# Kernel tuning notes

Hardware: AMD Instinct MI355X
Metric: run time of the kernel (lower is better)

Reference implementation:

```python
import jax, jax.numpy as jnp
import numpy as np

HEADS = 16
DIM_HEAD = 64
MAX_FREQ = 256.0  # lucidrains RotaryEmbedding(freqs_for='pixel', max_freq=256)


def axial_freqs(H, W, dim_head):
    # per-axis rotary dim = dim_head // 2 (RotaryEmbedding(dim=head_dim//2))
    d = dim_head // 2
    base = jnp.linspace(1.0, MAX_FREQ / 2.0, d // 2) * jnp.pi  # (d/2,)

    def axis(n):
        pos = jnp.linspace(-1.0, 1.0, n)              # pixel positions
        f = pos[:, None] * base                        # (n, d/2)
        return jnp.repeat(f, 2, axis=-1)               # (n, d) interleaved pairs

    fh = jnp.broadcast_to(axis(H)[:, None, :], (H, W, d))
    fw = jnp.broadcast_to(axis(W)[None, :, :], (H, W, d))
    return jnp.concatenate([fh, fw], axis=-1)          # (H, W, dim_head)


def apply_rope(t, freqs):
    # t: (B,T,H,W,h,d); freqs: (H,W,d)
    f = freqs[:, :, None, :]                           # broadcast over heads
    x = t.reshape(t.shape[:-1] + (t.shape[-1] // 2, 2))
    x1, x2 = x[..., 0], x[..., 1]
    rot = jnp.stack([-x2, x1], axis=-1).reshape(t.shape)  # rotate_half (interleaved)
    return t * jnp.cos(f) + rot * jnp.sin(f)


def setup_inputs() -> dict:
    key = jax.random.key(0)
    k1, k2, k3 = jax.random.split(key, 3)
    B, T, H, W, D = 1, 8, 32, 32, 1024
    inner = HEADS * DIM_HEAD
    x = jax.random.normal(k1, (B, T, H, W, D), dtype=jnp.float32)
    Wqkv = jax.random.normal(k2, (D, 3 * inner), dtype=jnp.float32) * 0.02
    Wout = jax.random.normal(k3, (inner, D), dtype=jnp.float32) * 0.02
    bout = jnp.zeros((D,), dtype=jnp.float32)
    return {"x": x, "Wqkv": Wqkv, "Wout": Wout, "bout": bout}


def reference(x, Wqkv, Wout, bout):
    B, T, H, W, D = x.shape
    qkv = x @ Wqkv                                     # (B,T,H,W,3*inner)
    q, k, v = jnp.split(qkv, 3, axis=-1)
    shp = (B, T, H, W, HEADS, DIM_HEAD)
    q, k, v = q.reshape(shp), k.reshape(shp), v.reshape(shp)
    freqs = axial_freqs(H, W, DIM_HEAD)
    q = apply_rope(q, freqs)
    k = apply_rope(k, freqs)
    S = H * W
    q = q.reshape(B * T, S, HEADS, DIM_HEAD)
    k = k.reshape(B * T, S, HEADS, DIM_HEAD)
    v = v.reshape(B * T, S, HEADS, DIM_HEAD)
    scale = 1.0 / np.sqrt(DIM_HEAD).astype(np.float32)
    att = jnp.einsum('bshd,bthd->bhst', q, k) * scale  # (BT, h, S, S)
    att = jax.nn.softmax(att, axis=-1)
    o = jnp.einsum('bhst,bthd->bshd', att, v)          # (BT, S, h, d)
    o = o.reshape(B, T, H, W, HEADS * DIM_HEAD)
    return o @ Wout + bout
```

## Files before the change

kernel.cpp:

```cpp
#include <hip/hip_runtime.h>
#include <math.h>

#define DMODEL 1024
#define NQKV   3072
#define SEQ    1024
#define NH     16
#define DH     64
#define HS     (SEQ*DH)
constexpr float PI_F   = 3.14159265358979323846f;
constexpr float LOG2E  = 1.44269504088896f;

typedef _Float16 half8   __attribute__((ext_vector_type(8)));
typedef _Float16 half4   __attribute__((ext_vector_type(4)));
typedef float    floatx4 __attribute__((ext_vector_type(4)));

__device__ __forceinline__ void gload_lds16(const _Float16* g, _Float16* l) {
    __builtin_amdgcn_global_load_lds(
        (const __attribute__((address_space(1))) unsigned int*)g,
        (__attribute__((address_space(3)))       unsigned int*)l,
        16, 0, 0);
}

__global__ __launch_bounds__(256) void cvt_f16(
    const float* __restrict__ in, _Float16* __restrict__ out, int n)
{
    int i = (blockIdx.x*256 + threadIdx.x)*8;
    if (i >= n) return;
    float4 a = *(const float4*)(in + i);
    float4 b = *(const float4*)(in + i + 4);
    half8 h;
    h[0]=(_Float16)a.x; h[1]=(_Float16)a.y; h[2]=(_Float16)a.z; h[3]=(_Float16)a.w;
    h[4]=(_Float16)b.x; h[5]=(_Float16)b.y; h[6]=(_Float16)b.z; h[7]=(_Float16)b.w;
    *(half8*)(out + i) = h;
}

__global__ __launch_bounds__(256) void tr_cvt(
    const float* __restrict__ in, _Float16* __restrict__ out, int R, int C)
{
    __shared__ float T[32][33];
    const int bx = blockIdx.x, by = blockIdx.y;
    const int tx = threadIdx.x & 31, ty = threadIdx.x >> 5;
#pragma unroll
    for (int i = 0; i < 4; ++i)
        T[ty + i*8][tx] = in[(size_t)(by*32 + ty + i*8)*C + bx*32 + tx];
    __syncthreads();
#pragma unroll
    for (int i = 0; i < 4; ++i)
        out[(size_t)(bx*32 + ty + i*8)*R + by*32 + tx] = (_Float16)T[tx][ty + i*8];
}

__global__ __launch_bounds__(512) void gemm1_f16(
    const _Float16* __restrict__ A, const _Float16* __restrict__ Bt,
    _Float16* __restrict__ C, int M, int N, int K)
{
    __shared__ _Float16 As[2][2][4096] __attribute__((aligned(16)));
    __shared__ _Float16 Bs[2][2][8192] __attribute__((aligned(16)));

    const int tid  = threadIdx.x;
    const int w    = tid >> 6, lane = tid & 63, quad = lane >> 4, l = lane & 15;
    const int wm   = (w >> 2)*64, wn = (w & 3)*64;

    int bid = blockIdx.y*gridDim.x + blockIdx.x;
    const int per = (gridDim.x*gridDim.y) >> 3;
    bid = (bid & 7)*per + (bid >> 3);
    const int bx = bid % gridDim.x, by = bid / gridDim.x;
    const int m0 = by*128, n0 = bx*256;

    const int rs   = tid >> 2;
    const int csrc = (tid & 3) ^ ((tid >> 3) & 3);
    const _Float16* ga = A  + (size_t)(m0 + rs)*K + csrc*8;
    const _Float16* gb = Bt + (size_t)(n0 + rs)*K + csrc*8;
    const int swz8 = (quad ^ ((l >> 1) & 3))*8;

    floatx4 acc[4][4];
#pragma unroll
    for (int i = 0; i < 4; ++i)
#pragma unroll
        for (int j = 0; j < 4; ++j)
#pragma unroll
            for (int r = 0; r < 4; ++r) acc[i][j][r] = 0.f;

    gload_lds16(ga,                        &As[0][0][w*512]);
    gload_lds16(gb,                        &Bs[0][0][w*512]);
    gload_lds16(gb + (size_t)128*K,        &Bs[0][0][4096 + w*512]);
    gload_lds16(ga + 32,                   &As[0][1][w*512]);
    gload_lds16(gb + 32,                   &Bs[0][1][w*512]);
    gload_lds16(gb + 32 + (size_t)128*K,   &Bs[0][1][4096 + w*512]);

    const int KT = K / 64;
    for (int kt = 0; kt < KT; ++kt) {
        const int cur = kt & 1, nxt = cur ^ 1;
        const bool pf = (kt + 1 < KT);
        const size_t ko = (size_t)(kt + 1)*64;
        half8 af[4], bf[4];

        if (pf) gload_lds16(ga + ko, &As[nxt][0][w*512]);
        if (pf) { asm volatile("s_waitcnt vmcnt(4)" ::: "memory"); }
        else    { asm volatile("s_waitcnt vmcnt(3)" ::: "memory"); }
        __builtin_amdgcn_s_barrier();
        __builtin_amdgcn_sched_barrier(0);
#pragma unroll
        for (int mt = 0; mt < 4; ++mt)
            af[mt] = *(half8*)&As[cur][0][(wm + mt*16 + l)*32 + swz8];
#pragma unroll
        for (int nt = 0; nt < 4; ++nt)
            bf[nt] = *(half8*)&Bs[cur][0][(wn + nt*16 + l)*32 + swz8];
        if (pf) {
            gload_lds16(gb + ko,                 &Bs[nxt][0][w*512]);
            gload_lds16(gb + ko + (size_t)128*K, &Bs[nxt][0][4096 + w*512]);
        }
        asm volatile("s_waitcnt lgkmcnt(0)" ::: "memory");
        __builtin_amdgcn_sched_barrier(0);
        __builtin_amdgcn_s_setprio(1);
#pragma unroll
        for (int mt = 0; mt < 4; ++mt)
#pragma unroll
            for (int nt = 0; nt < 4; ++nt)
                acc[mt][nt] = __builtin_amdgcn_mfma_f32_16x16x32_f16(af[mt], bf[nt], acc[mt][nt], 0, 0, 0);
        __builtin_amdgcn_s_setprio(0);

        if (pf) gload_lds16(ga + ko + 32, &As[nxt][1][w*512]);
        if (pf) { asm volatile("s_waitcnt vmcnt(4)" ::: "memory"); }
        else    { asm volatile("s_waitcnt vmcnt(0)" ::: "memory"); }
        __builtin_amdgcn_s_barrier();
        __builtin_amdgcn_sched_barrier(0);
#pragma unroll
        for (int mt = 0; mt < 4; ++mt)
            af[mt] = *(half8*)&As[cur][1][(wm + mt*16 + l)*32 + swz8];
#pragma unroll
        for (int nt = 0; nt < 4; ++nt)
            bf[nt] = *(half8*)&Bs[cur][1][(wn + nt*16 + l)*32 + swz8];
        if (pf) {
            gload_lds16(gb + ko + 32,                 &Bs[nxt][1][w*512]);
            gload_lds16(gb + ko + 32 + (size_t)128*K, &Bs[nxt][1][4096 + w*512]);
        }
        asm volatile("s_waitcnt lgkmcnt(0)" ::: "memory");
        __builtin_amdgcn_sched_barrier(0);
        __builtin_amdgcn_s_setprio(1);
#pragma unroll
        for (int mt = 0; mt < 4; ++mt)
#pragma unroll
            for (int nt = 0; nt < 4; ++nt)
                acc[mt][nt] = __builtin_amdgcn_mfma_f32_16x16x32_f16(af[mt], bf[nt], acc[mt][nt], 0, 0, 0);
        __builtin_amdgcn_s_setprio(0);
    }

#pragma unroll
    for (int mt = 0; mt < 4; ++mt)
#pragma unroll
        for (int r = 0; r < 4; ++r) {
            size_t row = m0 + wm + mt*16 + quad*4 + r;
#pragma unroll
            for (int nt = 0; nt < 4; ++nt)
                C[row*N + n0 + wn + nt*16 + l] = (_Float16)acc[mt][nt][r];
        }
}

__global__ __launch_bounds__(512) void gemm2_f16(
    const _Float16* __restrict__ A, const _Float16* __restrict__ Bt,
    const float* __restrict__ bias, float* __restrict__ C, int M, int N, int K)
{
    __shared__ _Float16 As[2][2][4096] __attribute__((aligned(16)));
    __shared__ _Float16 Bs[2][2][8192] __attribute__((aligned(16)));

    const int tid  = threadIdx.x;
    const int w    = tid >> 6, lane = tid & 63, quad = lane >> 4, l = lane & 15;
    const int wm   = (w >> 2)*64, wn = (w & 3)*64;

    int bid = blockIdx.y*gridDim.x + blockIdx.x;
    const int per = (gridDim.x*gridDim.y) >> 3;
    bid = (bid & 7)*per + (bid >> 3);
    const int bx = bid % gridDim.x, by = bid / gridDim.x;
    const int m0 = by*128, n0 = bx*256;

    const int rs   = tid >> 2;
    const int csrc = (tid & 3) ^ ((tid >> 3) & 3);
    const _Float16* ga = A  + (size_t)(m0 + rs)*K + csrc*8;
    const _Float16* gb = Bt + (size_t)(n0 + rs)*K + csrc*8;
    const int swz8 = (quad ^ ((l >> 1) & 3))*8;

    floatx4 acc[4][4];
#pragma unroll
    for (int i = 0; i < 4; ++i)
#pragma unroll
        for (int j = 0; j < 4; ++j)
#pragma unroll
            for (int r = 0; r < 4; ++r) acc[i][j][r] = 0.f;

    gload_lds16(ga,                        &As[0][0][w*512]);
    gload_lds16(gb,                        &Bs[0][0][w*512]);
    gload_lds16(gb + (size_t)128*K,        &Bs[0][0][4096 + w*512]);
    gload_lds16(ga + 32,                   &As[0][1][w*512]);
    gload_lds16(gb + 32,                   &Bs[0][1][w*512]);
    gload_lds16(gb + 32 + (size_t)128*K,   &Bs[0][1][4096 + w*512]);

    const int KT = K / 64;
    for (int kt = 0; kt < KT; ++kt) {
        const int cur = kt & 1, nxt = cur ^ 1;
        const bool pf = (kt + 1 < KT);
        const size_t ko = (size_t)(kt + 1)*64;
        half8 af[4], bf[4];

        if (pf) gload_lds16(ga + ko, &As[nxt][0][w*512]);
        if (pf) { asm volatile("s_waitcnt vmcnt(4)" ::: "memory"); }
        else    { asm volatile("s_waitcnt vmcnt(3)" ::: "memory"); }
        __builtin_amdgcn_s_barrier();
        __builtin_amdgcn_sched_barrier(0);
#pragma unroll
        for (int mt = 0; mt < 4; ++mt)
            af[mt] = *(half8*)&As[cur][0][(wm + mt*16 + l)*32 + swz8];
#pragma unroll
        for (int nt = 0; nt < 4; ++nt)
            bf[nt] = *(half8*)&Bs[cur][0][(wn + nt*16 + l)*32 + swz8];
        if (pf) {
            gload_lds16(gb + ko,                 &Bs[nxt][0][w*512]);
            gload_lds16(gb + ko + (size_t)128*K, &Bs[nxt][0][4096 + w*512]);
        }
        asm volatile("s_waitcnt lgkmcnt(0)" ::: "memory");
        __builtin_amdgcn_sched_barrier(0);
        __builtin_amdgcn_s_setprio(1);
#pragma unroll
        for (int mt = 0; mt < 4; ++mt)
#pragma unroll
            for (int nt = 0; nt < 4; ++nt)
                acc[mt][nt] = __builtin_amdgcn_mfma_f32_16x16x32_f16(af[mt], bf[nt], acc[mt][nt], 0, 0, 0);
        __builtin_amdgcn_s_setprio(0);

        if (pf) gload_lds16(ga + ko + 32, &As[nxt][1][w*512]);
        if (pf) { asm volatile("s_waitcnt vmcnt(4)" ::: "memory"); }
        else    { asm volatile("s_waitcnt vmcnt(0)" ::: "memory"); }
        __builtin_amdgcn_s_barrier();
        __builtin_amdgcn_sched_barrier(0);
#pragma unroll
        for (int mt = 0; mt < 4; ++mt)
            af[mt] = *(half8*)&As[cur][1][(wm + mt*16 + l)*32 + swz8];
#pragma unroll
        for (int nt = 0; nt < 4; ++nt)
            bf[nt] = *(half8*)&Bs[cur][1][(wn + nt*16 + l)*32 + swz8];
        if (pf) {
            gload_lds16(gb + ko + 32,                 &Bs[nxt][1][w*512]);
            gload_lds16(gb + ko + 32 + (size_t)128*K, &Bs[nxt][1][4096 + w*512]);
        }
        asm volatile("s_waitcnt lgkmcnt(0)" ::: "memory");
        __builtin_amdgcn_sched_barrier(0);
        __builtin_amdgcn_s_setprio(1);
#pragma unroll
        for (int mt = 0; mt < 4; ++mt)
#pragma unroll
            for (int nt = 0; nt < 4; ++nt)
                acc[mt][nt] = __builtin_amdgcn_mfma_f32_16x16x32_f16(af[mt], bf[nt], acc[mt][nt], 0, 0, 0);
        __builtin_amdgcn_s_setprio(0);
    }

#pragma unroll
    for (int mt = 0; mt < 4; ++mt)
#pragma unroll
        for (int r = 0; r < 4; ++r) {
            size_t row = m0 + wm + mt*16 + quad*4 + r;
#pragma unroll
            for (int nt = 0; nt < 4; ++nt) {
                int col = n0 + wn + nt*16 + l;
                C[row*N + col] = acc[mt][nt][r] + bias[col];
            }
        }
}

__global__ __launch_bounds__(256) void rope_scatter(
    const _Float16* __restrict__ qkv,
    _Float16* __restrict__ qw, _Float16* __restrict__ kw,
    _Float16* __restrict__ vt)
{
    const int sc = blockIdx.x;
    const int bh = blockIdx.y;
    const int bt = bh >> 4, head = bh & 15;
    const int s0 = sc*64;
    const int tid = threadIdx.x;
    const int d0 = (tid & 7)*8;

    __shared__ _Float16 T[64][80];

#pragma unroll
    for (int half = 0; half < 2; ++half) {
        const int r = (tid >> 3) + half*32;
        const int s = s0 + r;
        const _Float16* src = qkv + (size_t)(bt*SEQ + s)*NQKV + head*DH + d0;
        half8 hq = *(const half8*)(src);
        half8 hk = *(const half8*)(src + DMODEL);
        half8 hv = *(const half8*)(src + 2*DMODEL);
        float fq[8], fk[8];
#pragma unroll
        for (int j = 0; j < 8; ++j) { fq[j] = (float)hq[j]; fk[j] = (float)hk[j]; }
        const int hp = s >> 5, wp = s & 31;
        const float ph = -1.0f + hp*(2.0f/31.0f);
        const float pw = -1.0f + wp*(2.0f/31.0f);
#pragma unroll
        for (int p = 0; p < 4; ++p) {
            int pg = (d0 >> 1) + p;
            float pos = (pg < 16) ? ph : pw;
            int   gi  = (pg < 16) ? pg : (pg - 16);
            float th  = pos * ((1.0f + gi*(127.0f/15.0f)) * PI_F);
            float sn, cs;
            sincosf(th, &sn, &cs);
            float q1 = fq[2*p], q2 = fq[2*p+1];
            fq[2*p]   = q1*cs - q2*sn;
            fq[2*p+1] = q2*cs + q1*sn;
            float k1 = fk[2*p], k2 = fk[2*p+1];
            fk[2*p]   = k1*cs - k2*sn;
            fk[2*p+1] = k2*cs + k1*sn;
        }
        half8 oq, ok;
        const float qsc = 0.125f * LOG2E;
#pragma unroll
        for (int j = 0; j < 8; ++j) {
            oq[j] = (_Float16)(fq[j]*qsc);
            ok[j] = (_Float16)fk[j];
        }
        *(half8*)(qw + (size_t)bh*HS + (size_t)s*DH + d0) = oq;
        *(half8*)(kw + (size_t)bh*HS + (size_t)s*DH + d0) = ok;
#pragma unroll
        for (int j = 0; j < 8; ++j) T[d0 + j][r] = hv[j];
    }
    __syncthreads();
    const int d = tid >> 2, so = (tid & 3)*16;
    half8 v0 = *(half8*)&T[d][so];
    half8 v1 = *(half8*)&T[d][so + 8];
    _Float16* dst = vt + (size_t)bh*HS + (size_t)d*SEQ + s0 + so;
    *(half8*)dst       = v0;
    *(half8*)(dst + 8) = v1;
}

#define BC  64
#define LDH 68

__global__ __launch_bounds__(256) void attn_mfma(
    const _Float16* __restrict__ qw, const _Float16* __restrict__ kw,
    const _Float16* __restrict__ vt, _Float16* __restrict__ om)
{
    const int qc = blockIdx.x;
    const int bh = blockIdx.y;
    const int tid  = threadIdx.x;
    const int w    = tid >> 6;
    const int lane = tid & 63;
    const int quad = lane >> 4;
    const int l    = lane & 15;

    __shared__ _Float16 Ks[2][BC][LDH];
    __shared__ _Float16 Vs[2][DH][LDH];
    __shared__ _Float16 Ps[4][32][LDH];
    __shared__ float    Ls[4][32];

    const _Float16* qp = qw + (size_t)bh*HS + (size_t)(qc*128 + w*32)*DH;
    const _Float16* kp = kw + (size_t)bh*HS;
    const _Float16* vp = vt + (size_t)bh*HS;

    half8 qf[2][2];
#pragma unroll
    for (int qt = 0; qt < 2; ++qt) {
        qf[qt][0] = *(const half8*)(qp + (size_t)(qt*16 + l)*DH + quad*8);
        qf[qt][1] = *(const half8*)(qp + (size_t)(qt*16 + l)*DH + quad*8 + 32);
    }

    const int rs = tid >> 3;
    const int cs = (tid & 7)*8;

    half8 kr0 = *(const half8*)(kp + (size_t)rs*DH + cs);
    half8 kr1 = *(const half8*)(kp + (size_t)(rs+32)*DH + cs);
    half8 vr0 = *(const half8*)(vp + (size_t)rs*SEQ + cs);
    half8 vr1 = *(const half8*)(vp + (size_t)(rs+32)*SEQ + cs);
    *(half8*)&Ks[0][rs][cs]    = kr0;
    *(half8*)&Ks[0][rs+32][cs] = kr1;
    *(half8*)&Vs[0][rs][cs]    = vr0;
    *(half8*)&Vs[0][rs+32][cs] = vr1;

    floatx4 Of[2][4];
#pragma unroll
    for (int qt = 0; qt < 2; ++qt)
#pragma unroll
        for (int dt = 0; dt < 4; ++dt)
#pragma unroll
            for (int r = 0; r < 4; ++r) Of[qt][dt][r] = 0.f;
    float lsum[2] = {0.f, 0.f};

    __syncthreads();

    for (int kc = 0; kc < SEQ/BC; ++kc) {
        const int cur = kc & 1;
        if (kc < SEQ/BC - 1) {
            const _Float16* kn = kp + (size_t)(kc+1)*BC*DH;
            const _Float16* vn = vp + (size_t)(kc+1)*BC;
            kr0 = *(const half8*)(kn + (size_t)rs*DH + cs);
            kr1 = *(const half8*)(kn + (size_t)(rs+32)*DH + cs);
            vr0 = *(const half8*)(vn + (size_t)rs*SEQ + cs);
            vr1 = *(const half8*)(vn + (size_t)(rs+32)*SEQ + cs);
        }

        floatx4 Sf[2][4];
#pragma unroll
        for (int kg = 0; kg < 4; ++kg) {
            half8 af0 = *(half8*)&Ks[cur][kg*16 + l][quad*8];
            half8 af1 = *(half8*)&Ks[cur][kg*16 + l][quad*8 + 32];
#pragma unroll
            for (int qt = 0; qt < 2; ++qt) {
                floatx4 a;
#pragma unroll
                for (int r = 0; r < 4; ++r) a[r] = 0.f;
                a = __builtin_amdgcn_mfma_f32_16x16x32_f16(af0, qf[qt][0], a, 0, 0, 0);
                a = __builtin_amdgcn_mfma_f32_16x16x32_f16(af1, qf[qt][1], a, 0, 0, 0);
                Sf[qt][kg] = a;
            }
        }
#pragma unroll
        for (int qt = 0; qt < 2; ++qt)
#pragma unroll
            for (int kg = 0; kg < 4; ++kg) {
                half4 p4;
#pragma unroll
                for (int r = 0; r < 4; ++r) {
                    float p = __builtin_amdgcn_exp2f(Sf[qt][kg][r]);
                    lsum[qt] += p;
                    p4[r] = (_Float16)p;
                }
                *(half4*)&Ps[w][qt*16 + l][kg*16 + quad*4] = p4;
            }
        half8 pa[2][2];
#pragma unroll
        for (int qt = 0; qt < 2; ++qt) {
            pa[qt][0] = *(half8*)&Ps[w][qt*16 + l][quad*8];
            pa[qt][1] = *(half8*)&Ps[w][qt*16 + l][quad*8 + 32];
        }
#pragma unroll
        for (int dt = 0; dt < 4; ++dt) {
            half8 vb0 = *(half8*)&Vs[cur][dt*16 + l][quad*8];
            half8 vb1 = *(half8*)&Vs[cur][dt*16 + l][quad*8 + 32];
#pragma unroll
            for (int qt = 0; qt < 2; ++qt) {
                Of[qt][dt] = __builtin_amdgcn_mfma_f32_16x16x32_f16(pa[qt][0], vb0, Of[qt][dt], 0, 0, 0);
                Of[qt][dt] = __builtin_amdgcn_mfma_f32_16x16x32_f16(pa[qt][1], vb1, Of[qt][dt], 0, 0, 0);
            }
        }

        if (kc < SEQ/BC - 1) {
            *(half8*)&Ks[1-cur][rs][cs]    = kr0;
            *(half8*)&Ks[1-cur][rs+32][cs] = kr1;
            *(half8*)&Vs[1-cur][rs][cs]    = vr0;
            *(half8*)&Vs[1-cur][rs+32][cs] = vr1;
        }
        __syncthreads();
    }

#pragma unroll
    for (int qt = 0; qt < 2; ++qt) {
        lsum[qt] += __shfl_xor(lsum[qt], 16);
        lsum[qt] += __shfl_xor(lsum[qt], 32);
        if (quad == 0) Ls[w][qt*16 + l] = lsum[qt];
    }
    const int bt = bh >> 4, head = bh & 15;
    _Float16* opf = om + (size_t)(bt*SEQ + qc*128 + w*32)*DMODEL + head*DH;
#pragma unroll
    for (int qt = 0; qt < 2; ++qt) {
        float inv[4];
#pragma unroll
        for (int r = 0; r < 4; ++r) inv[r] = 1.0f / Ls[w][qt*16 + quad*4 + r];
#pragma unroll
        for (int dt = 0; dt < 4; ++dt)
#pragma unroll
            for (int r = 0; r < 4; ++r)
                opf[(size_t)(qt*16 + quad*4 + r)*DMODEL + dt*16 + l] =
                    (_Float16)(Of[qt][dt][r]*inv[r]);
    }
}

extern "C" void kernel_launch(void* const* d_in, const int* in_sizes, int n_in,
                              void* d_out, int out_size, void* d_ws, size_t ws_size,
                              hipStream_t stream)
{
    const float* x    = (const float*)d_in[0];
    const float* Wqkv = (const float*)d_in[1];
    const float* Wout = (const float*)d_in[2];
    const float* bout = (const float*)d_in[3];
    float* out = (float*)d_out;

    _Float16* ws   = (_Float16*)d_ws;
    _Float16* Xh   = ws;
    _Float16* Wqkt = ws + 8388608;
    _Float16* Wot  = ws + 11534336;
    _Float16* qkvt = ws + 12582912;
    _Float16* qw   = ws + 37748736;
    _Float16* kw   = ws + 46137344;
    _Float16* vt   = ws + 54525952;
    _Float16* om   = qkvt;

    hipLaunchKernelGGL(cvt_f16, dim3(4096), dim3(256), 0, stream,
                       x, Xh, 8388608);
    hipLaunchKernelGGL(tr_cvt, dim3(96, 32), dim3(256), 0, stream,
                       Wqkv, Wqkt, 1024, 3072);
    hipLaunchKernelGGL(tr_cvt, dim3(32, 32), dim3(256), 0, stream,
                       Wout, Wot, 1024, 1024);
    hipLaunchKernelGGL(gemm1_f16, dim3(12, 64), dim3(512), 0, stream,
                       Xh, Wqkt, qkvt, 8192, NQKV, DMODEL);
    hipLaunchKernelGGL(rope_scatter, dim3(16, 128), dim3(256), 0, stream,
                       qkvt, qw, kw, vt);
    hipLaunchKernelGGL(attn_mfma, dim3(8, 128), dim3(256), 0, stream,
                       qw, kw, vt, om);
    hipLaunchKernelGGL(gemm2_f16, dim3(4, 64), dim3(512), 0, stream,
                       om, Wot, bout, out, 8192, DMODEL, DMODEL);
}
```

Baseline: 259.9 us.

## Enlarge GEMM1 M-tile to 256 and attention query tile to 256 rows

```diff
diff --git a/kernel.cpp b/kernel.cpp
--- a/kernel.cpp
+++ b/kernel.cpp
@@ -53,18 +53,18 @@
     const _Float16* __restrict__ A, const _Float16* __restrict__ Bt,
     _Float16* __restrict__ C, int M, int N, int K)
 {
-    __shared__ _Float16 As[2][2][4096] __attribute__((aligned(16)));
+    __shared__ _Float16 As[2][2][8192] __attribute__((aligned(16)));
     __shared__ _Float16 Bs[2][2][8192] __attribute__((aligned(16)));
 
     const int tid  = threadIdx.x;
     const int w    = tid >> 6, lane = tid & 63, quad = lane >> 4, l = lane & 15;
-    const int wm   = (w >> 2)*64, wn = (w & 3)*64;
+    const int wm   = (w >> 2)*128, wn = (w & 3)*64;
 
     int bid = blockIdx.y*gridDim.x + blockIdx.x;
     const int per = (gridDim.x*gridDim.y) >> 3;
     bid = (bid & 7)*per + (bid >> 3);
     const int bx = bid % gridDim.x, by = bid / gridDim.x;
-    const int m0 = by*128, n0 = bx*256;
+    const int m0 = by*256, n0 = bx*256;
 
     const int rs   = tid >> 2;
     const int csrc = (tid & 3) ^ ((tid >> 3) & 3);
@@ -72,31 +72,36 @@
     const _Float16* gb = Bt + (size_t)(n0 + rs)*K + csrc*8;
     const int swz8 = (quad ^ ((l >> 1) & 3))*8;
 
-    floatx4 acc[4][4];
-#pragma unroll
-    for (int i = 0; i < 4; ++i)
+    floatx4 acc[8][4];
+#pragma unroll
+    for (int i = 0; i < 8; ++i)
 #pragma unroll
         for (int j = 0; j < 4; ++j)
 #pragma unroll
             for (int r = 0; r < 4; ++r) acc[i][j][r] = 0.f;
 
-    gload_lds16(ga,                        &As[0][0][w*512]);
-    gload_lds16(gb,                        &Bs[0][0][w*512]);
-    gload_lds16(gb + (size_t)128*K,        &Bs[0][0][4096 + w*512]);
-    gload_lds16(ga + 32,                   &As[0][1][w*512]);
-    gload_lds16(gb + 32,                   &Bs[0][1][w*512]);
-    gload_lds16(gb + 32 + (size_t)128*K,   &Bs[0][1][4096 + w*512]);
+    gload_lds16(ga,                      &As[0][0][w*512]);
+    gload_lds16(ga + (size_t)128*K,      &As[0][0][4096 + w*512]);
+    gload_lds16(gb,                      &Bs[0][0][w*512]);
+    gload_lds16(gb + (size_t)128*K,      &Bs[0][0][4096 + w*512]);
+    gload_lds16(ga + 32,                 &As[0][1][w*512]);
+    gload_lds16(ga + 32 + (size_t)128*K, &As[0][1][4096 + w*512]);
+    gload_lds16(gb + 32,                 &Bs[0][1][w*512]);
+    gload_lds16(gb + 32 + (size_t)128*K, &Bs[0][1][4096 + w*512]);
 
     const int KT = K / 64;
     for (int kt = 0; kt < KT; ++kt) {
         const int cur = kt & 1, nxt = cur ^ 1;
         const bool pf = (kt + 1 < KT);
         const size_t ko = (size_t)(kt + 1)*64;
-        half8 af[4], bf[4];
-
-        if (pf) gload_lds16(ga + ko, &As[nxt][0][w*512]);
-        if (pf) { asm volatile("s_waitcnt vmcnt(4)" ::: "memory"); }
-        else    { asm volatile("s_waitcnt vmcnt(3)" ::: "memory"); }
+        half8 af[8], bf[4];
+
+        if (pf) {
+            gload_lds16(ga + ko,                 &As[nxt][0][w*512]);
+            gload_lds16(ga + ko + (size_t)128*K, &As[nxt][0][4096 + w*512]);
+        }
+        if (pf) { asm volatile("s_waitcnt vmcnt(6)" ::: "memory"); }
+        else    { asm volatile("s_waitcnt vmcnt(4)" ::: "memory"); }
         __builtin_amdgcn_s_barrier();
         __builtin_amdgcn_sched_barrier(0);
 #pragma unroll
@@ -105,11 +110,15 @@
 #pragma unroll
         for (int nt = 0; nt < 4; ++nt)
             bf[nt] = *(half8*)&Bs[cur][0][(wn + nt*16 + l)*32 + swz8];
+        __builtin_amdgcn_sched_barrier(0);
+#pragma unroll
+        for (int mt = 4; mt < 8; ++mt)
+            af[mt] = *(half8*)&As[cur][0][(wm + mt*16 + l)*32 + swz8];
         if (pf) {
             gload_lds16(gb + ko,                 &Bs[nxt][0][w*512]);
             gload_lds16(gb + ko + (size_t)128*K, &Bs[nxt][0][4096 + w*512]);
         }
-        asm volatile("s_waitcnt lgkmcnt(0)" ::: "memory");
+        asm volatile("s_waitcnt lgkmcnt(4)" ::: "memory");
         __builtin_amdgcn_sched_barrier(0);
         __builtin_amdgcn_s_setprio(1);
 #pragma unroll
@@ -118,9 +127,21 @@
             for (int nt = 0; nt < 4; ++nt)
                 acc[mt][nt] = __builtin_amdgcn_mfma_f32_16x16x32_f16(af[mt], bf[nt], acc[mt][nt], 0, 0, 0);
         __builtin_amdgcn_s_setprio(0);
-
-        if (pf) gload_lds16(ga + ko + 32, &As[nxt][1][w*512]);
-        if (pf) { asm volatile("s_waitcnt vmcnt(4)" ::: "memory"); }
+        asm volatile("s_waitcnt lgkmcnt(0)" ::: "memory");
+        __builtin_amdgcn_sched_barrier(0);
+        __builtin_amdgcn_s_setprio(1);
+#pragma unroll
+        for (int mt = 4; mt < 8; ++mt)
+#pragma unroll
+            for (int nt = 0; nt < 4; ++nt)
+                acc[mt][nt] = __builtin_amdgcn_mfma_f32_16x16x32_f16(af[mt], bf[nt], acc[mt][nt], 0, 0, 0);
+        __builtin_amdgcn_s_setprio(0);
+
+        if (pf) {
+            gload_lds16(ga + ko + 32,                 &As[nxt][1][w*512]);
+            gload_lds16(ga + ko + 32 + (size_t)128*K, &As[nxt][1][4096 + w*512]);
+        }
+        if (pf) { asm volatile("s_waitcnt vmcnt(6)" ::: "memory"); }
         else    { asm volatile("s_waitcnt vmcnt(0)" ::: "memory"); }
         __builtin_amdgcn_s_barrier();
         __builtin_amdgcn_sched_barrier(0);
@@ -130,11 +151,15 @@
 #pragma unroll
         for (int nt = 0; nt < 4; ++nt)
             bf[nt] = *(half8*)&Bs[cur][1][(wn + nt*16 + l)*32 + swz8];
+        __builtin_amdgcn_sched_barrier(0);
+#pragma unroll
+        for (int mt = 4; mt < 8; ++mt)
+            af[mt] = *(half8*)&As[cur][1][(wm + mt*16 + l)*32 + swz8];
         if (pf) {
             gload_lds16(gb + ko + 32,                 &Bs[nxt][1][w*512]);
             gload_lds16(gb + ko + 32 + (size_t)128*K, &Bs[nxt][1][4096 + w*512]);
         }
-        asm volatile("s_waitcnt lgkmcnt(0)" ::: "memory");
+        asm volatile("s_waitcnt lgkmcnt(4)" ::: "memory");
         __builtin_amdgcn_sched_barrier(0);
         __builtin_amdgcn_s_setprio(1);
 #pragma unroll
@@ -143,10 +168,19 @@
             for (int nt = 0; nt < 4; ++nt)
                 acc[mt][nt] = __builtin_amdgcn_mfma_f32_16x16x32_f16(af[mt], bf[nt], acc[mt][nt], 0, 0, 0);
         __builtin_amdgcn_s_setprio(0);
-    }
-
-#pragma unroll
-    for (int mt = 0; mt < 4; ++mt)
+        asm volatile("s_waitcnt lgkmcnt(0)" ::: "memory");
+        __builtin_amdgcn_sched_barrier(0);
+        __builtin_amdgcn_s_setprio(1);
+#pragma unroll
+        for (int mt = 4; mt < 8; ++mt)
+#pragma unroll
+            for (int nt = 0; nt < 4; ++nt)
+                acc[mt][nt] = __builtin_amdgcn_mfma_f32_16x16x32_f16(af[mt], bf[nt], acc[mt][nt], 0, 0, 0);
+        __builtin_amdgcn_s_setprio(0);
+    }
+
+#pragma unroll
+    for (int mt = 0; mt < 8; ++mt)
 #pragma unroll
         for (int r = 0; r < 4; ++r) {
             size_t row = m0 + wm + mt*16 + quad*4 + r;
@@ -346,16 +380,16 @@
 
     __shared__ _Float16 Ks[2][BC][LDH];
     __shared__ _Float16 Vs[2][DH][LDH];
-    __shared__ _Float16 Ps[4][32][LDH];
-    __shared__ float    Ls[4][32];
-
-    const _Float16* qp = qw + (size_t)bh*HS + (size_t)(qc*128 + w*32)*DH;
+    __shared__ _Float16 Ps[4][64][LDH];
+    __shared__ float    Ls[4][64];
+
+    const _Float16* qp = qw + (size_t)bh*HS + (size_t)(qc*256 + w*64)*DH;
     const _Float16* kp = kw + (size_t)bh*HS;
     const _Float16* vp = vt + (size_t)bh*HS;
 
-    half8 qf[2][2];
-#pragma unroll
-    for (int qt = 0; qt < 2; ++qt) {
+    half8 qf[4][2];
+#pragma unroll
+    for (int qt = 0; qt < 4; ++qt) {
         qf[qt][0] = *(const half8*)(qp + (size_t)(qt*16 + l)*DH + quad*8);
         qf[qt][1] = *(const half8*)(qp + (size_t)(qt*16 + l)*DH + quad*8 + 32);
     }
@@ -372,14 +406,14 @@
     *(half8*)&Vs[0][rs][cs]    = vr0;
     *(half8*)&Vs[0][rs+32][cs] = vr1;
 
-    floatx4 Of[2][4];
-#pragma unroll
-    for (int qt = 0; qt < 2; ++qt)
+    floatx4 Of[4][4];
+#pragma unroll
+    for (int qt = 0; qt < 4; ++qt)
 #pragma unroll
         for (int dt = 0; dt < 4; ++dt)
 #pragma unroll
             for (int r = 0; r < 4; ++r) Of[qt][dt][r] = 0.f;
-    float lsum[2] = {0.f, 0.f};
+    float lsum[4] = {0.f, 0.f, 0.f, 0.f};
 
     __syncthreads();
 
@@ -394,37 +428,30 @@
             vr1 = *(const half8*)(vn + (size_t)(rs+32)*SEQ + cs);
         }
 
-        floatx4 Sf[2][4];
 #pragma unroll
         for (int kg = 0; kg < 4; ++kg) {
             half8 af0 = *(half8*)&Ks[cur][kg*16 + l][quad*8];
             half8 af1 = *(half8*)&Ks[cur][kg*16 + l][quad*8 + 32];
 #pragma unroll
-            for (int qt = 0; qt < 2; ++qt) {
+            for (int qt = 0; qt < 4; ++qt) {
                 floatx4 a;
 #pragma unroll
                 for (int r = 0; r < 4; ++r) a[r] = 0.f;
                 a = __builtin_amdgcn_mfma_f32_16x16x32_f16(af0, qf[qt][0], a, 0, 0, 0);
                 a = __builtin_amdgcn_mfma_f32_16x16x32_f16(af1, qf[qt][1], a, 0, 0, 0);
-                Sf[qt][kg] = a;
-            }
-        }
-#pragma unroll
-        for (int qt = 0; qt < 2; ++qt)
-#pragma unroll
-            for (int kg = 0; kg < 4; ++kg) {
                 half4 p4;
 #pragma unroll
                 for (int r = 0; r < 4; ++r) {
-                    float p = __builtin_amdgcn_exp2f(Sf[qt][kg][r]);
+                    float p = __builtin_amdgcn_exp2f(a[r]);
                     lsum[qt] += p;
                     p4[r] = (_Float16)p;
                 }
                 *(half4*)&Ps[w][qt*16 + l][kg*16 + quad*4] = p4;
             }
-        half8 pa[2][2];
-#pragma unroll
-        for (int qt = 0; qt < 2; ++qt) {
+        }
+        half8 pa[4][2];
+#pragma unroll
+        for (int qt = 0; qt < 4; ++qt) {
             pa[qt][0] = *(half8*)&Ps[w][qt*16 + l][quad*8];
             pa[qt][1] = *(half8*)&Ps[w][qt*16 + l][quad*8 + 32];
         }
@@ -433,7 +460,7 @@
             half8 vb0 = *(half8*)&Vs[cur][dt*16 + l][quad*8];
             half8 vb1 = *(half8*)&Vs[cur][dt*16 + l][quad*8 + 32];
 #pragma unroll
-            for (int qt = 0; qt < 2; ++qt) {
+            for (int qt = 0; qt < 4; ++qt) {
                 Of[qt][dt] = __builtin_amdgcn_mfma_f32_16x16x32_f16(pa[qt][0], vb0, Of[qt][dt], 0, 0, 0);
                 Of[qt][dt] = __builtin_amdgcn_mfma_f32_16x16x32_f16(pa[qt][1], vb1, Of[qt][dt], 0, 0, 0);
             }
@@ -449,15 +476,15 @@
     }
 
 #pragma unroll
-    for (int qt = 0; qt < 2; ++qt) {
+    for (int qt = 0; qt < 4; ++qt) {
         lsum[qt] += __shfl_xor(lsum[qt], 16);
         lsum[qt] += __shfl_xor(lsum[qt], 32);
         if (quad == 0) Ls[w][qt*16 + l] = lsum[qt];
     }
     const int bt = bh >> 4, head = bh & 15;
-    _Float16* opf = om + (size_t)(bt*SEQ + qc*128 + w*32)*DMODEL + head*DH;
-#pragma unroll
-    for (int qt = 0; qt < 2; ++qt) {
+    _Float16* opf = om + (size_t)(bt*SEQ + qc*256 + w*64)*DMODEL + head*DH;
+#pragma unroll
+    for (int qt = 0; qt < 4; ++qt) {
         float inv[4];
 #pragma unroll
         for (int r = 0; r < 4; ++r) inv[r] = 1.0f / Ls[w][qt*16 + quad*4 + r];
@@ -496,11 +523,11 @@
                        Wqkv, Wqkt, 1024, 3072);
     hipLaunchKernelGGL(tr_cvt, dim3(32, 32), dim3(256), 0, stream,
                        Wout, Wot, 1024, 1024);
-    hipLaunchKernelGGL(gemm1_f16, dim3(12, 64), dim3(512), 0, stream,
+    hipLaunchKernelGGL(gemm1_f16, dim3(12, 32), dim3(512), 0, stream,
                        Xh, Wqkt, qkvt, 8192, NQKV, DMODEL);
     hipLaunchKernelGGL(rope_scatter, dim3(16, 128), dim3(256), 0, stream,
                        qkvt, qw, kw, vt);
-    hipLaunchKernelGGL(attn_mfma, dim3(8, 128), dim3(256), 0, stream,
+    hipLaunchKernelGGL(attn_mfma, dim3(4, 128), dim3(256), 0, stream,
                        qw, kw, vt, om);
     hipLaunchKernelGGL(gemm2_f16, dim3(4, 64), dim3(512), 0, stream,
                        om, Wot, bout, out, 8192, DMODEL, DMODEL);
```

Measured after the change: 263.9 us. Within noise of the previous version (+1.6%).
